# Performance work log

Hardware: AMD Instinct MI355X
Metric: run time of the kernel (lower is better)

The kernel has to match this reference:

```python
import jax, jax.numpy as jnp
import numpy as np

N_NODES = 100000
N_EDGES = 1600000
D_IN, D_HID, D_OUT = 256, 128, 64


def setup_inputs() -> dict:
    key = jax.random.key(0)
    k = jax.random.split(key, 6)
    x = jax.random.normal(k[0], (N_NODES, D_IN), dtype=jnp.float32)
    edge_index = jax.random.randint(k[1], (2, N_EDGES), 0, N_NODES, dtype=jnp.int64)
    W1 = jax.random.normal(k[2], (D_IN, D_HID), dtype=jnp.float32) / np.sqrt(D_IN)
    b1 = jnp.zeros((D_HID,), dtype=jnp.float32)
    W2 = jax.random.normal(k[3], (D_HID, D_OUT), dtype=jnp.float32) / np.sqrt(D_HID)
    b2 = jnp.zeros((D_OUT,), dtype=jnp.float32)
    return {"x": x, "edge_index": edge_index, "W1": W1, "b1": b1, "W2": W2, "b2": b2}


def gcn_conv(x, W, b, src, dst, n):
    """PyG GCNConv: h = D^-1/2 (A+I) D^-1/2 (x W) + b, symmetric norm with self-loops."""
    h = x @ W                                           # [n, d_out]
    # degree from destination (col) index, +1 for the self-loop edge weight
    deg = jnp.ones((n,), x.dtype).at[dst].add(jnp.float32(1.0))
    dinv = jax.lax.rsqrt(deg)                           # deg >= 1, no inf
    norm = dinv[src] * dinv[dst]                        # [E]
    agg = jax.ops.segment_sum(h[src] * norm[:, None], dst, num_segments=n)
    agg = agg + h * (dinv * dinv)[:, None]              # self-loop contribution
    return agg + b


def reference(x, edge_index, W1, b1, W2, b2):
    src, dst = edge_index[0], edge_index[1]
    n = x.shape[0]
    h = gcn_conv(x, W1, b1, src, dst, n)
    h = jax.nn.relu(h)                                  # dropout is identity in eval mode
    out = gcn_conv(h, W2, b2, src, dst, n)
    return out
```

## Files before the change

### kernel.cpp

```cpp
#include <hip/hip_runtime.h>
#include <stdint.h>

typedef unsigned short u16;
typedef unsigned int u32;
typedef __bf16 bf16x8 __attribute__((ext_vector_type(8)));
typedef float floatx4 __attribute__((ext_vector_type(4)));

static __device__ __forceinline__ float bf2f(u16 u) {
  union { u32 i; float f; } v; v.i = ((u32)u) << 16; return v.f;
}
static __device__ __forceinline__ u16 f2bf(float f) {
  union { float f; u32 i; } v; v.f = f;
  u32 u = v.i;
  return (u16)((u + 0x7fffu + ((u >> 16) & 1u)) >> 16);
}

static __device__ __forceinline__ void gload_lds16(const void* g, void* l) {
  __builtin_amdgcn_global_load_lds(
      (const __attribute__((address_space(1))) void*)g,
      (__attribute__((address_space(3))) void*)l, 16, 0, 0);
}

__global__ void k_edgemode(const int* __restrict__ ei, int* __restrict__ flag) {
  int t = threadIdx.x;
  int v = ei[2 * t + 1];
  unsigned long long b = __ballot(v == 0);
  if (t == 0) *flag = (b == ~0ull) ? 1 : 0;
}

static __device__ __forceinline__ int edge_src(const int* ei, int E, int i, int m64) {
  return m64 ? ei[2 * (size_t)i] : ei[i];
}
static __device__ __forceinline__ int edge_dst(const int* ei, int E, int i, int m64) {
  return m64 ? ei[2 * (size_t)E + 2 * (size_t)i] : ei[(size_t)E + i];
}

__global__ void k_transpose(const float* __restrict__ W1, const float* __restrict__ W2,
                            u16* __restrict__ Wt1, u16* __restrict__ Wt2) {
  int i = blockIdx.x * 256 + threadIdx.x;
  if (i < 256 * 128) {
    int k = i >> 7, c = i & 127;
    Wt1[c * 256 + k] = f2bf(W1[i]);
  } else {
    int j = i - 256 * 128;
    if (j < 128 * 64) {
      int k = j >> 6, c = j & 63;
      Wt2[c * 128 + k] = f2bf(W2[j]);
    }
  }
}

#define CHUNK 2048

__global__ void k_count(const int* __restrict__ ei, int E, const int* __restrict__ flag,
                        int* __restrict__ bucket_cnt, int NB) {
  __shared__ int h[1024];
  const int t = threadIdx.x;
  for (int i = t; i < 1024; i += 256) h[i] = 0;
  __syncthreads();
  const int c0 = blockIdx.x * CHUNK;
  const int cnt = min(CHUNK, E - c0);
  const int m64 = *flag;
  for (int i = t; i < cnt; i += 256)
    atomicAdd(&h[edge_dst(ei, E, c0 + i, m64) >> 7], 1);
  __syncthreads();
  for (int i = t; i < NB; i += 256)
    if (h[i]) atomicAdd(&bucket_cnt[i], h[i]);
}

__global__ void k_bscan(const int* __restrict__ bucket_cnt, int* __restrict__ bucket_base,
                        int* __restrict__ bucket_cursor, int NB,
                        int* __restrict__ row_ptr, int n, int E) {
  __shared__ int ts[256];
  const int t = threadIdx.x;
  const int b4 = t * 4;
  int a0 = (b4 + 0 < NB) ? bucket_cnt[b4 + 0] : 0;
  int a1 = (b4 + 1 < NB) ? bucket_cnt[b4 + 1] : 0;
  int a2 = (b4 + 2 < NB) ? bucket_cnt[b4 + 2] : 0;
  int a3 = (b4 + 3 < NB) ? bucket_cnt[b4 + 3] : 0;
  int p1 = a0, p2 = p1 + a1, p3 = p2 + a2, tsum = p3 + a3;
  ts[t] = tsum;
  __syncthreads();
  for (int off = 1; off < 256; off <<= 1) {
    int x = (t >= off) ? ts[t - off] : 0;
    __syncthreads();
    ts[t] += x;
    __syncthreads();
  }
  int ex0 = ts[t] - tsum;
  int e[4] = {ex0, ex0 + p1, ex0 + p2, ex0 + p3};
#pragma unroll
  for (int j = 0; j < 4; ++j) {
    int i = b4 + j;
    if (i < NB) { bucket_base[i] = e[j]; bucket_cursor[i] = e[j]; }
  }
  if (t == 0) row_ptr[n] = E;
}

__global__ void k_place(const int* __restrict__ ei, int E, const int* __restrict__ flag,
                        int* __restrict__ bucket_cursor, uint2* __restrict__ pairs, int NB) {
  __shared__ int h[1024];
  __shared__ int ex[1024];
  __shared__ int cur[1024];
  __shared__ int ts[256];
  __shared__ uint2 stage[CHUNK];
  const int t = threadIdx.x;
  const int c0 = blockIdx.x * CHUNK;
  const int cnt = min(CHUNK, E - c0);
  const int m64 = *flag;

  for (int i = t; i < 1024; i += 256) h[i] = 0;
  __syncthreads();

  int es[8], ed[8];
#pragma unroll
  for (int j = 0; j < 8; ++j) {
    int i = t + j * 256;
    es[j] = 0; ed[j] = -1;
    if (i < cnt) {
      es[j] = edge_src(ei, E, c0 + i, m64);
      ed[j] = edge_dst(ei, E, c0 + i, m64);
      atomicAdd(&h[ed[j] >> 7], 1);
    }
  }
  __syncthreads();

  const int b4 = t * 4;
  int a0 = h[b4], a1 = h[b4 + 1], a2 = h[b4 + 2], a3 = h[b4 + 3];
  int p1 = a0, p2 = p1 + a1, p3 = p2 + a2, tsum = p3 + a3;
  ts[t] = tsum;
  __syncthreads();
  for (int off = 1; off < 256; off <<= 1) {
    int x = (t >= off) ? ts[t - off] : 0;
    __syncthreads();
    ts[t] += x;
    __syncthreads();
  }
  int ex0 = ts[t] - tsum;
  ex[b4] = ex0;       cur[b4] = ex0;
  ex[b4 + 1] = ex0 + p1; cur[b4 + 1] = ex0 + p1;
  ex[b4 + 2] = ex0 + p2; cur[b4 + 2] = ex0 + p2;
  ex[b4 + 3] = ex0 + p3; cur[b4 + 3] = ex0 + p3;
  __syncthreads();

#pragma unroll
  for (int j = 0; j < 8; ++j) {
    if (ed[j] >= 0) {
      int b = ed[j] >> 7;
      int pos = atomicAdd(&cur[b], 1);
      stage[pos] = make_uint2((u32)es[j], (u32)ed[j]);
    }
  }
  __syncthreads();
  for (int i = t; i < NB; i += 256) {
    int c = h[i];
    if (c > 0) h[i] = atomicAdd(&bucket_cursor[i], c);
  }
  __syncthreads();

  for (int i = t; i < cnt; i += 256) {
    uint2 p = stage[i];
    int b = (int)(p.y >> 7);
    pairs[h[b] + (i - ex[b])] = p;
  }
}

#define BMAX 3072
__global__ void k_csr(const uint2* __restrict__ pairs, const int* __restrict__ bucket_cnt,
                      const int* __restrict__ bucket_base, int* __restrict__ row_ptr,
                      float* __restrict__ dinv, int* __restrict__ srcs, int n) {
  __shared__ int h[128], cur[128];
  __shared__ int lsrc[BMAX];
  const int b = blockIdx.x;
  const int t = threadIdx.x;
  const int cnt = bucket_cnt[b];
  const int base = bucket_base[b];

  if (t < 128) h[t] = 0;
  __syncthreads();
  for (int i = t; i < cnt; i += 256)
    atomicAdd(&h[pairs[base + i].y & 127], 1);
  __syncthreads();

  __shared__ int sc[128];
  int v = 0;
  if (t < 128) { v = h[t]; sc[t] = v; }
  __syncthreads();
  for (int off = 1; off < 128; off <<= 1) {
    int x = 0;
    if (t < 128 && t >= off) x = sc[t - off];
    __syncthreads();
    if (t < 128) sc[t] += x;
    __syncthreads();
  }
  if (t < 128) {
    int excl = sc[t] - v;
    cur[t] = excl;
    int node = b * 128 + t;
    if (node < n) {
      row_ptr[node] = base + excl;
      dinv[node] = rsqrtf(1.0f + (float)v);
    }
  }
  __syncthreads();

  for (int i = t; i < cnt; i += 256) {
    uint2 p = pairs[base + i];
    int pos = atomicAdd(&cur[p.y & 127], 1);
    if (pos < BMAX) lsrc[pos] = (int)p.x;
    else srcs[base + pos] = (int)p.x;
  }
  __syncthreads();
  const int lim = min(cnt, BMAX);
  for (int i = t; i < lim; i += 256) srcs[base + i] = lsrc[i];
}

template<int N, int K, int CHK, bool A_FP32>
__launch_bounds__(256, 4)
__global__ void k_gemm(const void* __restrict__ Ap, const u16* __restrict__ Wt,
                       const float* __restrict__ dinv, u16* __restrict__ G, int M)
{
  constexpr int ESZ  = A_FP32 ? 4 : 2;
  constexpr int BPR  = K * ESZ;
  constexpr int BPRC = CHK * ESZ;
  constexpr int RPI  = 1024 / BPRC;
  constexpr int NISS = 64 / RPI;
  constexpr int STRIDE = 1024 + 16;
  constexpr int NCH  = K / CHK;
  constexpr int KSC  = CHK / 32;
  constexpr int IPW  = NISS / 4;
  constexpr int LPR  = BPRC / 16;
  __shared__ char lds[NISS * STRIDE];
  const int t = threadIdx.x;
  const int wave = t >> 6, lane = t & 63;
  const int row0 = blockIdx.x * 64;

  const int wr = wave >> 1, wc = wave & 1;
  constexpr int NT = N / 32;
  const int lm = lane & 15, lq = lane >> 4;

  floatx4 acc[2][NT];
#pragma unroll
  for (int i = 0; i < 2; ++i)
#pragma unroll
    for (int j = 0; j < NT; ++j) acc[i][j] = (floatx4)(0.0f);

  const int arow = wr * 32 + lm;
  const int brow0 = wc * (N / 2) + lm;

  for (int kc = 0; kc < NCH; ++kc) {
    const int kb = kc * BPRC;

#pragma unroll
    for (int i = 0; i < IPW; ++i) {
      const int g = wave * IPW + i;
      int r0 = row0 + g * RPI;
      if (r0 < M) {
        if (r0 > M - RPI) r0 = M - RPI;
        const char* src = (const char*)Ap + (size_t)r0 * BPR + kb
                          + (lane / LPR) * BPR + (lane % LPR) * 16;
        gload_lds16(src, lds + g * STRIDE);
      }
    }
    __syncthreads();

#pragma unroll
    for (int ksl = 0; ksl < KSC; ++ksl) {
      const int ks = kc * KSC + ksl;
      bf16x8 a[2];
#pragma unroll
      for (int mt = 0; mt < 2; ++mt) {
        const int r = arow + mt * 16;
        const char* p = lds + (r / RPI) * STRIDE + (r % RPI) * BPRC
                        + (ksl * 32 + lq * 8) * ESZ;
        if constexpr (A_FP32) {
          float4 f0 = *(const float4*)p;
          float4 f1 = *(const float4*)(p + 16);
          bf16x8 av;
          av[0] = (__bf16)f0.x; av[1] = (__bf16)f0.y; av[2] = (__bf16)f0.z; av[3] = (__bf16)f0.w;
          av[4] = (__bf16)f1.x; av[5] = (__bf16)f1.y; av[6] = (__bf16)f1.z; av[7] = (__bf16)f1.w;
          a[mt] = av;
        } else {
          a[mt] = *(const bf16x8*)p;
        }
      }
      bf16x8 b[NT];
#pragma unroll
      for (int nt = 0; nt < NT; ++nt)
        b[nt] = *(const bf16x8*)(Wt + (size_t)(brow0 + nt * 16) * K + ks * 32 + lq * 8);
#pragma unroll
      for (int nt = 0; nt < NT; ++nt) {
        acc[0][nt] = __builtin_amdgcn_mfma_f32_16x16x32_bf16(a[0], b[nt], acc[0][nt], 0, 0, 0);
        acc[1][nt] = __builtin_amdgcn_mfma_f32_16x16x32_bf16(a[1], b[nt], acc[1][nt], 0, 0, 0);
      }
    }
    __syncthreads();
  }

  const int crow0 = row0 + wr * 32 + lq * 4;
#pragma unroll
  for (int mt = 0; mt < 2; ++mt) {
#pragma unroll
    for (int nt = 0; nt < NT; ++nt) {
      const int gc = wc * (N / 2) + nt * 16 + lm;
#pragma unroll
      for (int r = 0; r < 4; ++r) {
        const int gr = crow0 + mt * 16 + r;
        if (gr < M) G[(size_t)gr * N + gc] = f2bf(acc[mt][nt][r] * dinv[gr]);
      }
    }
  }
}

template<int F, bool RELU, bool OUT_BF16>
__global__ void k_agg(const u16* __restrict__ g, const int* __restrict__ row_ptr,
                      const int* __restrict__ srcs, const float* __restrict__ dinv,
                      const float* __restrict__ bias, void* __restrict__ outp, int n)
{
  const int node = blockIdx.x * 4 + (threadIdx.x >> 6);
  if (node >= n) return;
  const int lane = threadIdx.x & 63;
  constexpr int VPL = F / 64;
  const int col = lane * VPL;
  float a0 = 0.f, a1 = 0.f;

  if constexpr (VPL == 2) {
    u32 v = *(const u32*)(g + (size_t)node * F + col);
    a0 += bf2f((u16)v); a1 += bf2f((u16)(v >> 16));
  } else {
    a0 += bf2f(g[(size_t)node * F + col]);
  }

  int e = row_ptr[node];
  const int e1 = row_ptr[node + 1];
  for (; e + 8 <= e1; e += 8) {
    int s[8];
#pragma unroll
    for (int j = 0; j < 8; ++j) s[j] = srcs[e + j];
    if constexpr (VPL == 2) {
      u32 v[8];
#pragma unroll
      for (int j = 0; j < 8; ++j) v[j] = *(const u32*)(g + (size_t)s[j] * F + col);
#pragma unroll
      for (int j = 0; j < 8; ++j) {
        a0 += bf2f((u16)v[j]);
        a1 += bf2f((u16)(v[j] >> 16));
      }
    } else {
      float f[8];
#pragma unroll
      for (int j = 0; j < 8; ++j) f[j] = bf2f(g[(size_t)s[j] * F + col]);
#pragma unroll
      for (int j = 0; j < 8; ++j) a0 += f[j];
    }
  }
  for (; e < e1; ++e) {
    int s0 = srcs[e];
    if constexpr (VPL == 2) {
      u32 v = *(const u32*)(g + (size_t)s0 * F + col);
      a0 += bf2f((u16)v); a1 += bf2f((u16)(v >> 16));
    } else {
      a0 += bf2f(g[(size_t)s0 * F + col]);
    }
  }

  const float dv = dinv[node];
  float o0 = dv * a0 + bias[col];
  if (RELU) o0 = fmaxf(o0, 0.f);
  float o1 = 0.f;
  if constexpr (VPL == 2) {
    o1 = dv * a1 + bias[col + 1];
    if (RELU) o1 = fmaxf(o1, 0.f);
  }

  if constexpr (OUT_BF16) {
    u16* out = (u16*)outp;
    if constexpr (VPL == 2) {
      u32 pk = (u32)f2bf(o0) | ((u32)f2bf(o1) << 16);
      *(u32*)(out + (size_t)node * F + col) = pk;
    } else {
      out[(size_t)node * F + col] = f2bf(o0);
    }
  } else {
    float* out = (float*)outp;
    if constexpr (VPL == 2) {
      *(float2*)(out + (size_t)node * F + col) = make_float2(o0, o1);
    } else {
      out[(size_t)node * F + col] = o0;
    }
  }
}

extern "C" void kernel_launch(void* const* d_in, const int* in_sizes, int n_in,
                              void* d_out, int out_size, void* d_ws, size_t ws_size,
                              hipStream_t stream)
{
  const float* x  = (const float*)d_in[0];
  const int*   ei = (const int*)d_in[1];
  const float* W1 = (const float*)d_in[2];
  const float* b1 = (const float*)d_in[3];
  const float* W2 = (const float*)d_in[4];
  const float* b2 = (const float*)d_in[5];

  const int n = in_sizes[0] / 256;
  const int E = in_sizes[1] / 2;
  const int NB = (n + 127) >> 7;

  char* ws = (char*)d_ws;
  size_t off = 0;
  auto alloc = [&](size_t bytes) -> void* {
    void* p = ws + off;
    off = (off + bytes + 255) & ~(size_t)255;
    return p;
  };
  int*   row_ptr = (int*)alloc((size_t)(n + 1) * 4);
  int*   bcnt    = (int*)alloc(1024 * 4);
  int*   bbase   = (int*)alloc(1024 * 4);
  int*   bcur    = (int*)alloc(1024 * 4);
  int*   eflag   = (int*)alloc(256);
  float* dinv    = (float*)alloc((size_t)n * 4);
  u16*   Wt1     = (u16*)alloc(256 * 128 * 2);
  u16*   Wt2     = (u16*)alloc(128 * 64 * 2);
  uint2* pairs   = (uint2*)alloc((size_t)E * 8);
  int*   srcs    = (int*)alloc((size_t)E * 4);
  u16*   g1      = (u16*)alloc((size_t)n * 128 * 2);
  u16*   y1      = (u16*)alloc((size_t)n * 128 * 2);
  u16*   g2      = (u16*)alloc((size_t)n * 64 * 2);
  (void)ws_size; (void)n_in; (void)out_size;

  const int TB = 256;
  const int nbC = (E + CHUNK - 1) / CHUNK;

  hipMemsetAsync(bcnt, 0, 1024 * 4, stream);
  k_edgemode<<<1, 64, 0, stream>>>(ei, eflag);
  k_transpose<<<(256 * 128 + 128 * 64 + TB - 1) / TB, TB, 0, stream>>>(W1, W2, Wt1, Wt2);
  k_count<<<nbC, TB, 0, stream>>>(ei, E, eflag, bcnt, NB);
  k_bscan<<<1, TB, 0, stream>>>(bcnt, bbase, bcur, NB, row_ptr, n, E);
  k_place<<<nbC, TB, 0, stream>>>(ei, E, eflag, bcur, pairs, NB);
  k_csr<<<NB, TB, 0, stream>>>(pairs, bcnt, bbase, row_ptr, dinv, srcs, n);

  k_gemm<128, 256, 128, true><<<(n + 63) / 64, 256, 0, stream>>>(x, Wt1, dinv, g1, n);
  k_agg<128, true, true><<<(n + 3) / 4, 256, 0, stream>>>(g1, row_ptr, srcs, dinv, b1, y1, n);
  k_gemm<64, 128, 128, false><<<(n + 63) / 64, 256, 0, stream>>>(y1, Wt2, dinv, g2, n);
  k_agg<64, false, false><<<(n + 3) / 4, 256, 0, stream>>>(g2, row_ptr, srcs, dinv, b2, d_out, n);
}
```

Before: 415.2 us.

## Fold self-loops into CSR and stream edges across nodes per wave with double-buffered gathers

```diff
diff --git a/kernel.cpp b/kernel.cpp
--- a/kernel.cpp
+++ b/kernel.cpp
@@ -94,7 +94,7 @@
     int i = b4 + j;
     if (i < NB) { bucket_base[i] = e[j]; bucket_cursor[i] = e[j]; }
   }
-  if (t == 0) row_ptr[n] = E;
+  if (t == 0) row_ptr[n] = E + n;
 }
 
 __global__ void k_place(const int* __restrict__ ei, int E, const int* __restrict__ flag,
@@ -175,6 +175,7 @@
   const int t = threadIdx.x;
   const int cnt = bucket_cnt[b];
   const int base = bucket_base[b];
+  const int nbase = base + b * 128;
 
   if (t < 128) h[t] = 0;
   __syncthreads();
@@ -195,11 +196,14 @@
   }
   if (t < 128) {
     int excl = sc[t] - v;
-    cur[t] = excl;
+    cur[t] = excl + t + 1;
     int node = b * 128 + t;
     if (node < n) {
-      row_ptr[node] = base + excl;
+      row_ptr[node] = nbase + excl + t;
       dinv[node] = rsqrtf(1.0f + (float)v);
+      int sp = excl + t;
+      if (sp < BMAX) lsrc[sp] = node;
+      else srcs[nbase + sp] = node;
     }
   }
   __syncthreads();
@@ -208,11 +212,11 @@
     uint2 p = pairs[base + i];
     int pos = atomicAdd(&cur[p.y & 127], 1);
     if (pos < BMAX) lsrc[pos] = (int)p.x;
-    else srcs[base + pos] = (int)p.x;
-  }
-  __syncthreads();
-  const int lim = min(cnt, BMAX);
-  for (int i = t; i < lim; i += 256) srcs[base + i] = lsrc[i];
+    else srcs[nbase + pos] = (int)p.x;
+  }
+  __syncthreads();
+  const int lim = min(cnt + 128, BMAX);
+  for (int i = t; i < lim; i += 256) srcs[nbase + i] = lsrc[i];
 }
 
 template<int N, int K, int CHK, bool A_FP32>
@@ -312,83 +316,102 @@
   }
 }
 
-template<int F, bool RELU, bool OUT_BF16>
+template<int F, bool RELU, bool OUT_BF16, int NPW>
+__launch_bounds__(256, 4)
 __global__ void k_agg(const u16* __restrict__ g, const int* __restrict__ row_ptr,
                       const int* __restrict__ srcs, const float* __restrict__ dinv,
                       const float* __restrict__ bias, void* __restrict__ outp, int n)
 {
-  const int node = blockIdx.x * 4 + (threadIdx.x >> 6);
-  if (node >= n) return;
+  const int wid = blockIdx.x * 4 + (threadIdx.x >> 6);
+  const int n0 = wid * NPW;
+  if (n0 >= n) return;
+  const int n1 = min(n0 + NPW, n);
   const int lane = threadIdx.x & 63;
   constexpr int VPL = F / 64;
   const int col = lane * VPL;
+  const float b0 = bias[col];
+  const float b1 = (VPL == 2) ? bias[col + (VPL - 1)] : 0.f;
+
+  int e    = __builtin_amdgcn_readfirstlane(row_ptr[n0]);
+  int eEnd = __builtin_amdgcn_readfirstlane(row_ptr[n1]);
+  int cur  = n0;
+  int nb   = __builtin_amdgcn_readfirstlane(row_ptr[n0 + 1]);
+  float dv = dinv[n0];
   float a0 = 0.f, a1 = 0.f;
 
-  if constexpr (VPL == 2) {
-    u32 v = *(const u32*)(g + (size_t)node * F + col);
-    a0 += bf2f((u16)v); a1 += bf2f((u16)(v >> 16));
-  } else {
-    a0 += bf2f(g[(size_t)node * F + col]);
-  }
-
-  int e = row_ptr[node];
-  const int e1 = row_ptr[node + 1];
-  for (; e + 8 <= e1; e += 8) {
-    int s[8];
-#pragma unroll
-    for (int j = 0; j < 8; ++j) s[j] = srcs[e + j];
+  auto fin = [&]() {
+    float o0 = dv * a0 + b0;
+    if (RELU) o0 = fmaxf(o0, 0.f);
     if constexpr (VPL == 2) {
-      u32 v[8];
-#pragma unroll
-      for (int j = 0; j < 8; ++j) v[j] = *(const u32*)(g + (size_t)s[j] * F + col);
-#pragma unroll
-      for (int j = 0; j < 8; ++j) {
-        a0 += bf2f((u16)v[j]);
-        a1 += bf2f((u16)(v[j] >> 16));
+      float o1 = dv * a1 + b1;
+      if (RELU) o1 = fmaxf(o1, 0.f);
+      if constexpr (OUT_BF16) {
+        u32 pk = (u32)f2bf(o0) | ((u32)f2bf(o1) << 16);
+        *(u32*)((u16*)outp + (size_t)cur * F + col) = pk;
+      } else {
+        *(float2*)((float*)outp + (size_t)cur * F + col) = make_float2(o0, o1);
       }
     } else {
-      float f[8];
-#pragma unroll
-      for (int j = 0; j < 8; ++j) f[j] = bf2f(g[(size_t)s[j] * F + col]);
-#pragma unroll
-      for (int j = 0; j < 8; ++j) a0 += f[j];
-    }
-  }
-  for (; e < e1; ++e) {
-    int s0 = srcs[e];
-    if constexpr (VPL == 2) {
-      u32 v = *(const u32*)(g + (size_t)s0 * F + col);
-      a0 += bf2f((u16)v); a1 += bf2f((u16)(v >> 16));
-    } else {
-      a0 += bf2f(g[(size_t)s0 * F + col]);
-    }
-  }
-
-  const float dv = dinv[node];
-  float o0 = dv * a0 + bias[col];
-  if (RELU) o0 = fmaxf(o0, 0.f);
-  float o1 = 0.f;
-  if constexpr (VPL == 2) {
-    o1 = dv * a1 + bias[col + 1];
-    if (RELU) o1 = fmaxf(o1, 0.f);
-  }
-
-  if constexpr (OUT_BF16) {
-    u16* out = (u16*)outp;
-    if constexpr (VPL == 2) {
-      u32 pk = (u32)f2bf(o0) | ((u32)f2bf(o1) << 16);
-      *(u32*)(out + (size_t)node * F + col) = pk;
-    } else {
-      out[(size_t)node * F + col] = f2bf(o0);
-    }
-  } else {
-    float* out = (float*)outp;
-    if constexpr (VPL == 2) {
-      *(float2*)(out + (size_t)node * F + col) = make_float2(o0, o1);
-    } else {
-      out[(size_t)node * F + col] = o0;
-    }
-  }
+      if constexpr (OUT_BF16) ((u16*)outp)[(size_t)cur * F + col] = f2bf(o0);
+      else                    ((float*)outp)[(size_t)cur * F + col] = o0;
+    }
+    ++cur;
+    a0 = 0.f; a1 = 0.f;
+    if (cur < n) {
+      dv = dinv[cur];
+      nb = __builtin_amdgcn_readfirstlane(row_ptr[cur + 1]);
+    }
+  };
+
+  auto issue = [&](int eb, u32* gv) {
+    const int* sp = srcs + eb;
+#pragma unroll
+    for (int j = 0; j < 8; ++j) {
+      const int s = sp[j];
+      if constexpr (VPL == 2)
+        gv[j] = *(const u32*)(g + (size_t)s * F + col);
+      else
+        gv[j] = (u32)g[(size_t)s * F + col];
+    }
+  };
+
+  auto consume = [&](int eb, const u32* gv) {
+#pragma unroll
+    for (int j = 0; j < 8; ++j) {
+      if (eb + j == nb) fin();
+      if constexpr (VPL == 2) {
+        a0 += bf2f((u16)gv[j]);
+        a1 += bf2f((u16)(gv[j] >> 16));
+      } else {
+        a0 += bf2f((u16)gv[j]);
+      }
+    }
+  };
+
+  u32 gvA[8], gvB[8];
+  const int rem = (eEnd - e) >> 3;
+  if (rem >= 1) issue(e, gvA);
+  if (rem >= 2) issue(e + 8, gvB);
+  int i = 0;
+  for (; i + 2 < rem; i += 2) {
+    consume(e + i * 8, gvA);
+    issue(e + (i + 2) * 8, gvA);
+    consume(e + (i + 1) * 8, gvB);
+    if (i + 3 < rem) issue(e + (i + 3) * 8, gvB);
+  }
+  if (i < rem) { consume(e + i * 8, gvA); ++i; }
+  if (i < rem) { consume(e + i * 8, gvB); ++i; }
+
+  for (int et = e + rem * 8; et < eEnd; ++et) {
+    const int s = srcs[et];
+    u32 gvt;
+    if constexpr (VPL == 2) gvt = *(const u32*)(g + (size_t)s * F + col);
+    else                    gvt = (u32)g[(size_t)s * F + col];
+    if (et == nb) fin();
+    if constexpr (VPL == 2) { a0 += bf2f((u16)gvt); a1 += bf2f((u16)(gvt >> 16)); }
+    else                    a0 += bf2f((u16)gvt);
+  }
+  fin();
 }
 
 extern "C" void kernel_launch(void* const* d_in, const int* in_sizes, int n_in,
@@ -422,7 +445,7 @@
   u16*   Wt1     = (u16*)alloc(256 * 128 * 2);
   u16*   Wt2     = (u16*)alloc(128 * 64 * 2);
   uint2* pairs   = (uint2*)alloc((size_t)E * 8);
-  int*   srcs    = (int*)alloc((size_t)E * 4);
+  int*   srcs    = (int*)alloc((size_t)(E + n + 512) * 4);
   u16*   g1      = (u16*)alloc((size_t)n * 128 * 2);
   u16*   y1      = (u16*)alloc((size_t)n * 128 * 2);
   u16*   g2      = (u16*)alloc((size_t)n * 64 * 2);
@@ -439,8 +462,12 @@
   k_place<<<nbC, TB, 0, stream>>>(ei, E, eflag, bcur, pairs, NB);
   k_csr<<<NB, TB, 0, stream>>>(pairs, bcnt, bbase, row_ptr, dinv, srcs, n);
 
+  constexpr int NPW = 8;
+  const int nwaves = (n + NPW - 1) / NPW;
+  const int aggGrid = (nwaves + 3) / 4;
+
   k_gemm<128, 256, 128, true><<<(n + 63) / 64, 256, 0, stream>>>(x, Wt1, dinv, g1, n);
-  k_agg<128, true, true><<<(n + 3) / 4, 256, 0, stream>>>(g1, row_ptr, srcs, dinv, b1, y1, n);
+  k_agg<128, true, true, NPW><<<aggGrid, 256, 0, stream>>>(g1, row_ptr, srcs, dinv, b1, y1, n);
   k_gemm<64, 128, 128, false><<<(n + 63) / 64, 256, 0, stream>>>(y1, Wt2, dinv, g2, n);
-  k_agg<64, false, false><<<(n + 3) / 4, 256, 0, stream>>>(g2, row_ptr, srcs, dinv, b2, d_out, n);
-}
+  k_agg<64, false, false, NPW><<<aggGrid, 256, 0, stream>>>(g2, row_ptr, srcs, dinv, b2, d_out, n);
+}
```

Measured after the change: 381.2 us. 1.09x faster.
